# Kernel tuning notes

Hardware: AMD Instinct MI355X
Metric: run time of the kernel (lower is better)

The kernel has to match this reference:

```python
import jax, jax.numpy as jnp
import numpy as np

N, D, P = 16384, 128, 256  # rows, hidden_size, prompt_num


def setup_inputs() -> dict:
    key = jax.random.key(0)
    k1, k2 = jax.random.split(key)
    repres = jax.random.normal(k1, (N, D), dtype=jnp.float32)
    # learned memory bank parameter (torch uses xavier_normal with relu gain; scale is immaterial for correctness baseline)
    xavier_std = np.float32(np.sqrt(2.0) * np.sqrt(2.0 / (P + D)))
    memory = jax.random.normal(k2, (P, D), dtype=jnp.float32) * xavier_std
    return {"repres": repres, "memory": memory}


def _forward(repres, memory):
    hid = repres.shape[1]
    # attention over memory bank: [N, P]
    attention = jax.nn.softmax(jnp.einsum('nd,fd->nf', repres, memory), axis=1)
    # attention-weighted readout: [N, D]
    output = jnp.einsum('nf,fd->nd', attention, memory)
    # top-2 prototypes per row
    _, idx = jax.lax.top_k(attention, 2)           # idx: [N, 2]
    largest = memory[idx[:, 0]]                    # [N, D]
    second_largest = memory[idx[:, 1]]             # [N, D]
    distance1 = jnp.linalg.norm(repres - largest, axis=1) / hid
    distance2 = jnp.linalg.norm(repres - second_largest, axis=1) / hid
    loss_constraint = jnp.mean(distance1)
    diff = distance1 - distance2 + 0.001
    temp = diff < 0
    cnt = jnp.sum(temp)
    # mean over masked elements, only added when any element satisfies the mask
    loss2 = jnp.sum(jnp.where(temp, diff, 0.0)) / jnp.maximum(cnt, 1).astype(diff.dtype)
    loss_constraint = loss_constraint + jnp.where(cnt > 0, loss2, jnp.float32(0.0))
    # Frobenius norm of the memory bank
    loss_constraint = loss_constraint + jnp.linalg.norm(memory)
    out = jnp.concatenate([output, repres], axis=1)  # [N, 2D]
    top1 = idx[:, 0]
    same_proto_mask = top1[:, None] == top1[None, :]  # [N, N] bool
    return out, loss_constraint, same_proto_mask


def reference(repres, memory):
    return _forward(repres, memory)
```

## Files before the change

### kernel.cpp

```cpp
#include <hip/hip_runtime.h>
#include <math.h>

#define NROWS 16384
#define DIM   128
#define PROTO 256
#define ROWS_PER_BLK 16
#define MASK_ROWS_PER_BLK 64
#define MASK_BLOCKS (NROWS / MASK_ROWS_PER_BLK)

#define OUT_COLS 256
#define LOSS_OFF ((size_t)NROWS * OUT_COLS)
#define MASK_OFF (LOSS_OFF + 1)

typedef float f32x4 __attribute__((ext_vector_type(4)));
typedef float f32x2 __attribute__((ext_vector_type(2)));


__global__ __launch_bounds__(256) void transpose_mem(
    const float* __restrict__ memory, float* __restrict__ memT)
{
    __shared__ float tile[8][DIM + 1];
    const int t  = threadIdx.x;
    const int p0 = blockIdx.x * 8;
    #pragma unroll
    for (int k = 0; k < 4; ++k) {
        const int idx = t + k * 256;
        const int p = idx >> 7, d = idx & 127;
        tile[p][d] = memory[(size_t)(p0 + p) * DIM + d];
    }
    __syncthreads();
    #pragma unroll
    for (int k = 0; k < 4; ++k) {
        const int idx = t + k * 256;
        const int d = idx >> 3, p = idx & 7;
        memT[(size_t)d * PROTO + p0 + p] = tile[p][d];
    }
}

__global__ __launch_bounds__(256) void fused_rows(
    const float* __restrict__ repres,
    const float* __restrict__ memory,
    const float* __restrict__ memT,
    float* __restrict__ out,
    int*   __restrict__ top1w,
    float* __restrict__ d1w,
    float* __restrict__ negw,
    float* __restrict__ flagw)
{
    __shared__ float rep_lds[ROWS_PER_BLK * DIM];
    __shared__ float s_lds[ROWS_PER_BLK * PROTO];
    __shared__ float inv_lds[ROWS_PER_BLK];

    const int tid  = threadIdx.x;
    const int row0 = blockIdx.x * ROWS_PER_BLK;
    const int rg   = tid >> 6;
    const int lane = tid & 63;

    {
        const float4* src = (const float4*)(repres + (size_t)row0 * DIM);
        float4* dst = (float4*)rep_lds;
        dst[tid]       = src[tid];
        dst[tid + 256] = src[tid + 256];
    }

    {
        const int urg = __builtin_amdgcn_readfirstlane(rg);
        const float4* a0 = (const float4*)(repres + (size_t)(row0 + 4 * urg) * DIM);
        const f32x4*  bT = (const f32x4*)memT + lane;

        float acc[4][4];
        #pragma unroll
        for (int i = 0; i < 4; ++i)
            #pragma unroll
            for (int j = 0; j < 4; ++j) acc[i][j] = 0.f;

        for (int d4 = 0; d4 < DIM / 4; ++d4) {
            float4 a_[4];
            #pragma unroll
            for (int i = 0; i < 4; ++i) a_[i] = a0[i * (DIM / 4) + d4];
            f32x4 b_[4];
            #pragma unroll
            for (int k = 0; k < 4; ++k) b_[k] = bT[(4 * d4 + k) * (PROTO / 4)];
            #pragma unroll
            for (int i = 0; i < 4; ++i) {
                #pragma unroll
                for (int j = 0; j < 4; ++j) {
                    acc[i][j] = fmaf(a_[i].x, b_[0][j], acc[i][j]);
                    acc[i][j] = fmaf(a_[i].y, b_[1][j], acc[i][j]);
                    acc[i][j] = fmaf(a_[i].z, b_[2][j], acc[i][j]);
                    acc[i][j] = fmaf(a_[i].w, b_[3][j], acc[i][j]);
                }
            }
        }
        f32x4* s4 = (f32x4*)s_lds;
        #pragma unroll
        for (int i = 0; i < 4; ++i) {
            f32x4 v; v.x = acc[i][0]; v.y = acc[i][1]; v.z = acc[i][2]; v.w = acc[i][3];
            s4[(size_t)(4 * rg + i) * (PROTO / 4) + lane] = v;
        }
    }
    __syncthreads();

    {
        for (int q = 0; q < 4; ++q) {
            const int r = rg * 4 + q;
            float s[4]; int pidx[4];
            #pragma unroll
            for (int k = 0; k < 4; ++k) {
                pidx[k] = lane + 64 * k;
                s[k] = s_lds[r * PROTO + pidx[k]];
            }
            float mx = fmaxf(fmaxf(s[0], s[1]), fmaxf(s[2], s[3]));
            #pragma unroll
            for (int off = 1; off < 64; off <<= 1)
                mx = fmaxf(mx, __shfl_xor(mx, off, 64));
            float e[4], sum = 0.f;
            #pragma unroll
            for (int k = 0; k < 4; ++k) { e[k] = __expf(s[k] - mx); sum += e[k]; }
            #pragma unroll
            for (int off = 1; off < 64; off <<= 1)
                sum += __shfl_xor(sum, off, 64);
            #pragma unroll
            for (int k = 0; k < 4; ++k) s_lds[r * PROTO + pidx[k]] = e[k];

            float v1 = s[0], v2 = -INFINITY;
            int   i1 = pidx[0], i2 = 0x7fffffff;
            #pragma unroll
            for (int k = 1; k < 4; ++k) {
                float v = s[k]; int i = pidx[k];
                if (v > v1 || (v == v1 && i < i1)) { v2 = v1; i2 = i1; v1 = v; i1 = i; }
                else if (v > v2 || (v == v2 && i < i2)) { v2 = v; i2 = i; }
            }
            #pragma unroll
            for (int off = 1; off < 64; off <<= 1) {
                float ov1 = __shfl_xor(v1, off, 64), ov2 = __shfl_xor(v2, off, 64);
                int   oi1 = __shfl_xor(i1, off, 64), oi2 = __shfl_xor(i2, off, 64);
                if (ov1 > v1 || (ov1 == v1 && oi1 < i1)) { v2 = v1; i2 = i1; v1 = ov1; i1 = oi1; }
                else if (ov1 > v2 || (ov1 == v2 && oi1 < i2)) { v2 = ov1; i2 = oi1; }
                if (ov2 > v2 || (ov2 == v2 && oi2 < i2)) { v2 = ov2; i2 = oi2; }
            }

            const float rx = rep_lds[r * DIM + 2 * lane];
            const float ry = rep_lds[r * DIM + 2 * lane + 1];
            float dx = rx - memory[(size_t)i1 * DIM + 2 * lane];
            float dy = ry - memory[(size_t)i1 * DIM + 2 * lane + 1];
            float ss1 = dx * dx + dy * dy;
            dx = rx - memory[(size_t)i2 * DIM + 2 * lane];
            dy = ry - memory[(size_t)i2 * DIM + 2 * lane + 1];
            float ss2 = dx * dx + dy * dy;
            #pragma unroll
            for (int off = 1; off < 64; off <<= 1) {
                ss1 += __shfl_xor(ss1, off, 64);
                ss2 += __shfl_xor(ss2, off, 64);
            }
            if (lane == 0) {
                const int grow = row0 + r;
                float dist1 = sqrtf(ss1) / 128.f;
                float dist2 = sqrtf(ss2) / 128.f;
                top1w[grow] = i1;
                d1w[grow]   = dist1;
                float diff  = dist1 - dist2 + 0.001f;
                negw[grow]  = (diff < 0.f) ? diff : 0.f;
                flagw[grow] = (diff < 0.f) ? 1.f : 0.f;
                inv_lds[r]  = 1.0f / sum;
            }
        }
    }

    {
        const int d0 = 2 * lane;
        float accx[4], accy[4];
        #pragma unroll
        for (int i = 0; i < 4; ++i) { accx[i] = 0.f; accy[i] = 0.f; }

        const f32x4* s4 = (const f32x4*)s_lds;
        for (int p4 = 0; p4 < PROTO / 4; ++p4) {
            f32x4 e[4];
            #pragma unroll
            for (int i = 0; i < 4; ++i)
                e[i] = s4[(size_t)(4 * rg + i) * (PROTO / 4) + p4];
            #pragma unroll
            for (int k = 0; k < 4; ++k) {
                const f32x2 m2 = *(const f32x2*)(memory + (size_t)(p4 * 4 + k) * DIM + d0);
                #pragma unroll
                for (int i = 0; i < 4; ++i) {
                    accx[i] = fmaf(e[i][k], m2.x, accx[i]);
                    accy[i] = fmaf(e[i][k], m2.y, accy[i]);
                }
            }
        }
        #pragma unroll
        for (int i = 0; i < 4; ++i) {
            const int r = 4 * rg + i;
            const size_t grow = (size_t)(row0 + r);
            const float inv = inv_lds[r];
            f32x2 o; o.x = accx[i] * inv; o.y = accy[i] * inv;
            *(f32x2*)(out + grow * OUT_COLS + d0) = o;
            f32x2 rp; rp.x = rep_lds[r * DIM + d0]; rp.y = rep_lds[r * DIM + d0 + 1];
            *(f32x2*)(out + grow * OUT_COLS + 128 + d0) = rp;
        }
    }
}

__global__ __launch_bounds__(256) void mask_loss_kernel(
    const int* __restrict__ top1,
    const float* __restrict__ memory,
    const float* __restrict__ d1w,
    const float* __restrict__ negw,
    const float* __restrict__ flagw,
    float* __restrict__ out)
{
    const int b   = blockIdx.x;
    const int tid = threadIdx.x;

    if (b == MASK_BLOCKS) {
        __shared__ float red[4 * 256];
        float s1 = 0.f, s2 = 0.f, s3 = 0.f, s4 = 0.f;
        for (int q = tid; q < NROWS; q += 256) {
            s1 += d1w[q]; s2 += negw[q]; s3 += flagw[q];
        }
        for (int q = tid; q < PROTO * DIM; q += 256) {
            float v = memory[q];
            s4 = fmaf(v, v, s4);
        }
        red[tid] = s1; red[256 + tid] = s2; red[512 + tid] = s3; red[768 + tid] = s4;
        __syncthreads();
        for (int off = 128; off > 0; off >>= 1) {
            if (tid < off) {
                red[tid]       += red[tid + off];
                red[256 + tid] += red[256 + tid + off];
                red[512 + tid] += red[512 + tid + off];
                red[768 + tid] += red[768 + tid + off];
            }
            __syncthreads();
        }
        if (tid == 0) {
            float loss = red[0] / (float)NROWS;
            float cnt  = red[512];
            if (cnt > 0.f) loss += red[256] / cnt;
            loss += sqrtf(red[768]);
            out[LOSS_OFF] = loss;
        }
        return;
    }

    __shared__ unsigned int lds_u32[NROWS / 4];
    unsigned char* lds_u8 = (unsigned char*)lds_u32;
    {
        const int4* t4 = (const int4*)top1;
        #pragma unroll
        for (int k = 0; k < 16; ++k) {
            const int g = tid + (k << 8);
            const int4 a = t4[g];
            lds_u32[g] = (unsigned)(a.x & 255) | ((unsigned)(a.y & 255) << 8)
                       | ((unsigned)(a.z & 255) << 16) | ((unsigned)a.w << 24);
        }
    }
    __syncthreads();

    for (int rr = 0; rr < MASK_ROWS_PER_BLK; ++rr) {
        const int r = b * MASK_ROWS_PER_BLK + rr;
        const int ti = (int)lds_u8[r];
        float* __restrict__ row = out + MASK_OFF + (size_t)r * NROWS;

        if (tid < 31) {
            row[tid] = ((int)lds_u8[tid] == ti) ? 1.f : 0.f;
        } else if (tid == 31) {
            row[NROWS - 1] = ((int)lds_u8[NROWS - 1] == ti) ? 1.f : 0.f;
        }

        #pragma unroll 4
        for (int k = 0; k < 16; ++k) {
            const int h = tid + (k << 8);
            if (h < 4088) {
                const unsigned w0 = lds_u32[h + 7];
                const unsigned w1 = lds_u32[h + 8];
                const unsigned x  = (w0 >> 24) | (w1 << 8);
                f32x4 v;
                v.x = ((int)(x & 255)         == ti) ? 1.f : 0.f;
                v.y = ((int)((x >> 8) & 255)  == ti) ? 1.f : 0.f;
                v.z = ((int)((x >> 16) & 255) == ti) ? 1.f : 0.f;
                v.w = ((int)(x >> 24)         == ti) ? 1.f : 0.f;
                *(f32x4*)(row + 31 + (h << 2)) = v;
            }
        }
    }
}

extern "C" void kernel_launch(void* const* d_in, const int* in_sizes, int n_in,
                              void* d_out, int out_size, void* d_ws, size_t ws_size,
                              hipStream_t stream)
{
    const float* repres = (const float*)d_in[0];
    const float* memory = (const float*)d_in[1];
    float* out = (float*)d_out;

    int*   top1w = (int*)d_ws;
    float* fws   = (float*)d_ws;
    float* d1w   = fws + NROWS;
    float* negw  = fws + 2 * NROWS;
    float* flagw = fws + 3 * NROWS;
    float* memTw = fws + 4 * NROWS;

    transpose_mem<<<dim3(PROTO / 8), dim3(256), 0, stream>>>(memory, memTw);
    fused_rows<<<dim3(NROWS / ROWS_PER_BLK), dim3(256), 0, stream>>>(
        repres, memory, memTw, out, top1w, d1w, negw, flagw);
    mask_loss_kernel<<<dim3(MASK_BLOCKS + 1), dim3(256), 0, stream>>>(
        top1w, memory, d1w, negw, flagw, out);
}
```

Before: 301.4 us.

## Split top-k pass from readout and co-schedule readout with mask writes

The fused row kernel is split. A lighter top_kernel computes the scores, top-2 and distances, and the softmax readout and output writes move into a combined kernel alongside the mask and loss blocks. The goal is to overlap the compute-bound readout with the bandwidth-bound N×N mask writes in a single launch. The cost is that the score matmul now runs twice and repres is read twice.

```diff
diff --git a/kernel.cpp b/kernel.cpp
--- a/kernel.cpp
+++ b/kernel.cpp
@@ -7,6 +7,7 @@
 #define ROWS_PER_BLK 16
 #define MASK_ROWS_PER_BLK 64
 #define MASK_BLOCKS (NROWS / MASK_ROWS_PER_BLK)
+#define OUT_BLOCKS  (NROWS / ROWS_PER_BLK)
 
 #define OUT_COLS 256
 #define LOSS_OFF ((size_t)NROWS * OUT_COLS)
@@ -37,11 +38,10 @@
     }
 }
 
-__global__ __launch_bounds__(256) void fused_rows(
+__global__ __launch_bounds__(256) void top_kernel(
     const float* __restrict__ repres,
     const float* __restrict__ memory,
     const float* __restrict__ memT,
-    float* __restrict__ out,
     int*   __restrict__ top1w,
     float* __restrict__ d1w,
     float* __restrict__ negw,
@@ -49,7 +49,6 @@
 {
     __shared__ float rep_lds[ROWS_PER_BLK * DIM];
     __shared__ float s_lds[ROWS_PER_BLK * PROTO];
-    __shared__ float inv_lds[ROWS_PER_BLK];
 
     const int tid  = threadIdx.x;
     const int row0 = blockIdx.x * ROWS_PER_BLK;
@@ -101,70 +100,220 @@
     }
     __syncthreads();
 
-    {
-        for (int q = 0; q < 4; ++q) {
-            const int r = rg * 4 + q;
-            float s[4]; int pidx[4];
-            #pragma unroll
-            for (int k = 0; k < 4; ++k) {
-                pidx[k] = lane + 64 * k;
-                s[k] = s_lds[r * PROTO + pidx[k]];
-            }
-            float mx = fmaxf(fmaxf(s[0], s[1]), fmaxf(s[2], s[3]));
-            #pragma unroll
-            for (int off = 1; off < 64; off <<= 1)
-                mx = fmaxf(mx, __shfl_xor(mx, off, 64));
-            float e[4], sum = 0.f;
-            #pragma unroll
-            for (int k = 0; k < 4; ++k) { e[k] = __expf(s[k] - mx); sum += e[k]; }
-            #pragma unroll
-            for (int off = 1; off < 64; off <<= 1)
-                sum += __shfl_xor(sum, off, 64);
-            #pragma unroll
-            for (int k = 0; k < 4; ++k) s_lds[r * PROTO + pidx[k]] = e[k];
-
-            float v1 = s[0], v2 = -INFINITY;
-            int   i1 = pidx[0], i2 = 0x7fffffff;
-            #pragma unroll
-            for (int k = 1; k < 4; ++k) {
-                float v = s[k]; int i = pidx[k];
-                if (v > v1 || (v == v1 && i < i1)) { v2 = v1; i2 = i1; v1 = v; i1 = i; }
-                else if (v > v2 || (v == v2 && i < i2)) { v2 = v; i2 = i; }
-            }
-            #pragma unroll
-            for (int off = 1; off < 64; off <<= 1) {
-                float ov1 = __shfl_xor(v1, off, 64), ov2 = __shfl_xor(v2, off, 64);
-                int   oi1 = __shfl_xor(i1, off, 64), oi2 = __shfl_xor(i2, off, 64);
-                if (ov1 > v1 || (ov1 == v1 && oi1 < i1)) { v2 = v1; i2 = i1; v1 = ov1; i1 = oi1; }
-                else if (ov1 > v2 || (ov1 == v2 && oi1 < i2)) { v2 = ov1; i2 = oi1; }
-                if (ov2 > v2 || (ov2 == v2 && oi2 < i2)) { v2 = ov2; i2 = oi2; }
-            }
-
-            const float rx = rep_lds[r * DIM + 2 * lane];
-            const float ry = rep_lds[r * DIM + 2 * lane + 1];
-            float dx = rx - memory[(size_t)i1 * DIM + 2 * lane];
-            float dy = ry - memory[(size_t)i1 * DIM + 2 * lane + 1];
-            float ss1 = dx * dx + dy * dy;
-            dx = rx - memory[(size_t)i2 * DIM + 2 * lane];
-            dy = ry - memory[(size_t)i2 * DIM + 2 * lane + 1];
-            float ss2 = dx * dx + dy * dy;
-            #pragma unroll
-            for (int off = 1; off < 64; off <<= 1) {
-                ss1 += __shfl_xor(ss1, off, 64);
-                ss2 += __shfl_xor(ss2, off, 64);
-            }
-            if (lane == 0) {
-                const int grow = row0 + r;
-                float dist1 = sqrtf(ss1) / 128.f;
-                float dist2 = sqrtf(ss2) / 128.f;
-                top1w[grow] = i1;
-                d1w[grow]   = dist1;
-                float diff  = dist1 - dist2 + 0.001f;
-                negw[grow]  = (diff < 0.f) ? diff : 0.f;
-                flagw[grow] = (diff < 0.f) ? 1.f : 0.f;
-                inv_lds[r]  = 1.0f / sum;
-            }
-        }
+    for (int q = 0; q < 4; ++q) {
+        const int r = rg * 4 + q;
+        float s[4]; int pidx[4];
+        #pragma unroll
+        for (int k = 0; k < 4; ++k) {
+            pidx[k] = lane + 64 * k;
+            s[k] = s_lds[r * PROTO + pidx[k]];
+        }
+        float v1 = s[0], v2 = -INFINITY;
+        int   i1 = pidx[0], i2 = 0x7fffffff;
+        #pragma unroll
+        for (int k = 1; k < 4; ++k) {
+            float v = s[k]; int i = pidx[k];
+            if (v > v1 || (v == v1 && i < i1)) { v2 = v1; i2 = i1; v1 = v; i1 = i; }
+            else if (v > v2 || (v == v2 && i < i2)) { v2 = v; i2 = i; }
+        }
+        #pragma unroll
+        for (int off = 1; off < 64; off <<= 1) {
+            float ov1 = __shfl_xor(v1, off, 64), ov2 = __shfl_xor(v2, off, 64);
+            int   oi1 = __shfl_xor(i1, off, 64), oi2 = __shfl_xor(i2, off, 64);
+            if (ov1 > v1 || (ov1 == v1 && oi1 < i1)) { v2 = v1; i2 = i1; v1 = ov1; i1 = oi1; }
+            else if (ov1 > v2 || (ov1 == v2 && oi1 < i2)) { v2 = ov1; i2 = oi1; }
+            if (ov2 > v2 || (ov2 == v2 && oi2 < i2)) { v2 = ov2; i2 = oi2; }
+        }
+
+        const float rx = rep_lds[r * DIM + 2 * lane];
+        const float ry = rep_lds[r * DIM + 2 * lane + 1];
+        float dx = rx - memory[(size_t)i1 * DIM + 2 * lane];
+        float dy = ry - memory[(size_t)i1 * DIM + 2 * lane + 1];
+        float ss1 = dx * dx + dy * dy;
+        dx = rx - memory[(size_t)i2 * DIM + 2 * lane];
+        dy = ry - memory[(size_t)i2 * DIM + 2 * lane + 1];
+        float ss2 = dx * dx + dy * dy;
+        #pragma unroll
+        for (int off = 1; off < 64; off <<= 1) {
+            ss1 += __shfl_xor(ss1, off, 64);
+            ss2 += __shfl_xor(ss2, off, 64);
+        }
+        if (lane == 0) {
+            const int grow = row0 + r;
+            float dist1 = sqrtf(ss1) / 128.f;
+            float dist2 = sqrtf(ss2) / 128.f;
+            top1w[grow] = i1;
+            d1w[grow]   = dist1;
+            float diff  = dist1 - dist2 + 0.001f;
+            negw[grow]  = (diff < 0.f) ? diff : 0.f;
+            flagw[grow] = (diff < 0.f) ? 1.f : 0.f;
+        }
+    }
+}
+
+__global__ __launch_bounds__(256) void combo_kernel(
+    const float* __restrict__ repres,
+    const float* __restrict__ memory,
+    const float* __restrict__ memT,
+    const int* __restrict__ top1,
+    const float* __restrict__ d1w,
+    const float* __restrict__ negw,
+    const float* __restrict__ flagw,
+    float* __restrict__ out)
+{
+    const int b   = blockIdx.x;
+    const int tid = threadIdx.x;
+
+    if (b < MASK_BLOCKS) {
+        __shared__ unsigned int lds_u32[NROWS / 4];
+        unsigned char* lds_u8 = (unsigned char*)lds_u32;
+        {
+            const int4* t4 = (const int4*)top1;
+            #pragma unroll
+            for (int k = 0; k < 16; ++k) {
+                const int g = tid + (k << 8);
+                const int4 a = t4[g];
+                lds_u32[g] = (unsigned)(a.x & 255) | ((unsigned)(a.y & 255) << 8)
+                           | ((unsigned)(a.z & 255) << 16) | ((unsigned)a.w << 24);
+            }
+        }
+        __syncthreads();
+
+        for (int rr = 0; rr < MASK_ROWS_PER_BLK; ++rr) {
+            const int r = b * MASK_ROWS_PER_BLK + rr;
+            const int ti = (int)lds_u8[r];
+            float* __restrict__ row = out + MASK_OFF + (size_t)r * NROWS;
+
+            if (tid < 31) {
+                row[tid] = ((int)lds_u8[tid] == ti) ? 1.f : 0.f;
+            } else if (tid == 31) {
+                row[NROWS - 1] = ((int)lds_u8[NROWS - 1] == ti) ? 1.f : 0.f;
+            }
+
+            #pragma unroll 4
+            for (int k = 0; k < 16; ++k) {
+                const int h = tid + (k << 8);
+                if (h < 4088) {
+                    const unsigned w0 = lds_u32[h + 7];
+                    const unsigned w1 = lds_u32[h + 8];
+                    const unsigned x  = (w0 >> 24) | (w1 << 8);
+                    f32x4 v;
+                    v.x = ((int)(x & 255)         == ti) ? 1.f : 0.f;
+                    v.y = ((int)((x >> 8) & 255)  == ti) ? 1.f : 0.f;
+                    v.z = ((int)((x >> 16) & 255) == ti) ? 1.f : 0.f;
+                    v.w = ((int)(x >> 24)         == ti) ? 1.f : 0.f;
+                    *(f32x4*)(row + 31 + (h << 2)) = v;
+                }
+            }
+        }
+        return;
+    }
+
+    if (b == MASK_BLOCKS) {
+        __shared__ float red[4 * 256];
+        float s1 = 0.f, s2 = 0.f, s3 = 0.f, s4 = 0.f;
+        for (int q = tid; q < NROWS; q += 256) {
+            s1 += d1w[q]; s2 += negw[q]; s3 += flagw[q];
+        }
+        for (int q = tid; q < PROTO * DIM; q += 256) {
+            float v = memory[q];
+            s4 = fmaf(v, v, s4);
+        }
+        red[tid] = s1; red[256 + tid] = s2; red[512 + tid] = s3; red[768 + tid] = s4;
+        __syncthreads();
+        for (int off = 128; off > 0; off >>= 1) {
+            if (tid < off) {
+                red[tid]       += red[tid + off];
+                red[256 + tid] += red[256 + tid + off];
+                red[512 + tid] += red[512 + tid + off];
+                red[768 + tid] += red[768 + tid + off];
+            }
+            __syncthreads();
+        }
+        if (tid == 0) {
+            float loss = red[0] / (float)NROWS;
+            float cnt  = red[512];
+            if (cnt > 0.f) loss += red[256] / cnt;
+            loss += sqrtf(red[768]);
+            out[LOSS_OFF] = loss;
+        }
+        return;
+    }
+
+    __shared__ float rep_lds[ROWS_PER_BLK * DIM];
+    __shared__ float s_lds[ROWS_PER_BLK * PROTO];
+    __shared__ float inv_lds[ROWS_PER_BLK];
+
+    const int row0 = (b - MASK_BLOCKS - 1) * ROWS_PER_BLK;
+    const int rg   = tid >> 6;
+    const int lane = tid & 63;
+
+    {
+        const float4* src = (const float4*)(repres + (size_t)row0 * DIM);
+        float4* dst = (float4*)rep_lds;
+        dst[tid]       = src[tid];
+        dst[tid + 256] = src[tid + 256];
+    }
+
+    {
+        const int urg = __builtin_amdgcn_readfirstlane(rg);
+        const float4* a0 = (const float4*)(repres + (size_t)(row0 + 4 * urg) * DIM);
+        const f32x4*  bT = (const f32x4*)memT + lane;
+
+        float acc[4][4];
+        #pragma unroll
+        for (int i = 0; i < 4; ++i)
+            #pragma unroll
+            for (int j = 0; j < 4; ++j) acc[i][j] = 0.f;
+
+        for (int d4 = 0; d4 < DIM / 4; ++d4) {
+            float4 a_[4];
+            #pragma unroll
+            for (int i = 0; i < 4; ++i) a_[i] = a0[i * (DIM / 4) + d4];
+            f32x4 b_[4];
+            #pragma unroll
+            for (int k = 0; k < 4; ++k) b_[k] = bT[(4 * d4 + k) * (PROTO / 4)];
+            #pragma unroll
+            for (int i = 0; i < 4; ++i) {
+                #pragma unroll
+                for (int j = 0; j < 4; ++j) {
+                    acc[i][j] = fmaf(a_[i].x, b_[0][j], acc[i][j]);
+                    acc[i][j] = fmaf(a_[i].y, b_[1][j], acc[i][j]);
+                    acc[i][j] = fmaf(a_[i].z, b_[2][j], acc[i][j]);
+                    acc[i][j] = fmaf(a_[i].w, b_[3][j], acc[i][j]);
+                }
+            }
+        }
+        f32x4* s4 = (f32x4*)s_lds;
+        #pragma unroll
+        for (int i = 0; i < 4; ++i) {
+            f32x4 v; v.x = acc[i][0]; v.y = acc[i][1]; v.z = acc[i][2]; v.w = acc[i][3];
+            s4[(size_t)(4 * rg + i) * (PROTO / 4) + lane] = v;
+        }
+    }
+    __syncthreads();
+
+    for (int q = 0; q < 4; ++q) {
+        const int r = rg * 4 + q;
+        float s[4]; int pidx[4];
+        #pragma unroll
+        for (int k = 0; k < 4; ++k) {
+            pidx[k] = lane + 64 * k;
+            s[k] = s_lds[r * PROTO + pidx[k]];
+        }
+        float mx = fmaxf(fmaxf(s[0], s[1]), fmaxf(s[2], s[3]));
+        #pragma unroll
+        for (int off = 1; off < 64; off <<= 1)
+            mx = fmaxf(mx, __shfl_xor(mx, off, 64));
+        float e[4], sum = 0.f;
+        #pragma unroll
+        for (int k = 0; k < 4; ++k) { e[k] = __expf(s[k] - mx); sum += e[k]; }
+        #pragma unroll
+        for (int off = 1; off < 64; off <<= 1)
+            sum += __shfl_xor(sum, off, 64);
+        #pragma unroll
+        for (int k = 0; k < 4; ++k) s_lds[r * PROTO + pidx[k]] = e[k];
+        if (lane == 0) inv_lds[r] = 1.0f / sum;
     }
 
     {
@@ -202,91 +351,6 @@
     }
 }
 
-__global__ __launch_bounds__(256) void mask_loss_kernel(
-    const int* __restrict__ top1,
-    const float* __restrict__ memory,
-    const float* __restrict__ d1w,
-    const float* __restrict__ negw,
-    const float* __restrict__ flagw,
-    float* __restrict__ out)
-{
-    const int b   = blockIdx.x;
-    const int tid = threadIdx.x;
-
-    if (b == MASK_BLOCKS) {
-        __shared__ float red[4 * 256];
-        float s1 = 0.f, s2 = 0.f, s3 = 0.f, s4 = 0.f;
-        for (int q = tid; q < NROWS; q += 256) {
-            s1 += d1w[q]; s2 += negw[q]; s3 += flagw[q];
-        }
-        for (int q = tid; q < PROTO * DIM; q += 256) {
-            float v = memory[q];
-            s4 = fmaf(v, v, s4);
-        }
-        red[tid] = s1; red[256 + tid] = s2; red[512 + tid] = s3; red[768 + tid] = s4;
-        __syncthreads();
-        for (int off = 128; off > 0; off >>= 1) {
-            if (tid < off) {
-                red[tid]       += red[tid + off];
-                red[256 + tid] += red[256 + tid + off];
-                red[512 + tid] += red[512 + tid + off];
-                red[768 + tid] += red[768 + tid + off];
-            }
-            __syncthreads();
-        }
-        if (tid == 0) {
-            float loss = red[0] / (float)NROWS;
-            float cnt  = red[512];
-            if (cnt > 0.f) loss += red[256] / cnt;
-            loss += sqrtf(red[768]);
-            out[LOSS_OFF] = loss;
-        }
-        return;
-    }
-
-    __shared__ unsigned int lds_u32[NROWS / 4];
-    unsigned char* lds_u8 = (unsigned char*)lds_u32;
-    {
-        const int4* t4 = (const int4*)top1;
-        #pragma unroll
-        for (int k = 0; k < 16; ++k) {
-            const int g = tid + (k << 8);
-            const int4 a = t4[g];
-            lds_u32[g] = (unsigned)(a.x & 255) | ((unsigned)(a.y & 255) << 8)
-                       | ((unsigned)(a.z & 255) << 16) | ((unsigned)a.w << 24);
-        }
-    }
-    __syncthreads();
-
-    for (int rr = 0; rr < MASK_ROWS_PER_BLK; ++rr) {
-        const int r = b * MASK_ROWS_PER_BLK + rr;
-        const int ti = (int)lds_u8[r];
-        float* __restrict__ row = out + MASK_OFF + (size_t)r * NROWS;
-
-        if (tid < 31) {
-            row[tid] = ((int)lds_u8[tid] == ti) ? 1.f : 0.f;
-        } else if (tid == 31) {
-            row[NROWS - 1] = ((int)lds_u8[NROWS - 1] == ti) ? 1.f : 0.f;
-        }
-
-        #pragma unroll 4
-        for (int k = 0; k < 16; ++k) {
-            const int h = tid + (k << 8);
-            if (h < 4088) {
-                const unsigned w0 = lds_u32[h + 7];
-                const unsigned w1 = lds_u32[h + 8];
-                const unsigned x  = (w0 >> 24) | (w1 << 8);
-                f32x4 v;
-                v.x = ((int)(x & 255)         == ti) ? 1.f : 0.f;
-                v.y = ((int)((x >> 8) & 255)  == ti) ? 1.f : 0.f;
-                v.z = ((int)((x >> 16) & 255) == ti) ? 1.f : 0.f;
-                v.w = ((int)(x >> 24)         == ti) ? 1.f : 0.f;
-                *(f32x4*)(row + 31 + (h << 2)) = v;
-            }
-        }
-    }
-}
-
 extern "C" void kernel_launch(void* const* d_in, const int* in_sizes, int n_in,
                               void* d_out, int out_size, void* d_ws, size_t ws_size,
                               hipStream_t stream)
@@ -303,8 +367,8 @@
     float* memTw = fws + 4 * NROWS;
 
     transpose_mem<<<dim3(PROTO / 8), dim3(256), 0, stream>>>(memory, memTw);
-    fused_rows<<<dim3(NROWS / ROWS_PER_BLK), dim3(256), 0, stream>>>(
-        repres, memory, memTw, out, top1w, d1w, negw, flagw);
-    mask_loss_kernel<<<dim3(MASK_BLOCKS + 1), dim3(256), 0, stream>>>(
-        top1w, memory, d1w, negw, flagw, out);
+    top_kernel<<<dim3(NROWS / ROWS_PER_BLK), dim3(256), 0, stream>>>(
+        repres, memory, memTw, top1w, d1w, negw, flagw);
+    combo_kernel<<<dim3(MASK_BLOCKS + 1 + OUT_BLOCKS), dim3(256), 0, stream>>>(
+        repres, memory, memTw, top1w, d1w, negw, flagw, out);
 }
```

Result: faster. 259.4 us, median of 2 (-13.9%).
